# Kernel optimization log

Measured on AMD Instinct MI355X. Metric: run time of the kernel, lower is better.

## Reference

```python
import jax, jax.numpy as jnp
import numpy as np

DN = ('NHWC', 'HWIO', 'NHWC')
EPS = 1e-3  # Keras BatchNormalization default epsilon


def conv2d(x, w):
    return jax.lax.conv_general_dilated(x, w, (1, 1), 'SAME', dimension_numbers=DN)


def hard_sigmoid(x):
    # Keras ConvLSTM2D default recurrent_activation
    return jnp.clip(0.2 * x + 0.5, 0.0, 1.0)


def convlstm2d(x, Wx, Wh, b):
    """Keras ConvLSTM2D, return_sequences=True. x: (B,T,H,W,C).
    Wx: (3,3,C,4F) input kernel, Wh: (3,3,F,4F) recurrent kernel, b: (4F,).
    Gate order (Keras): i, f, c, o."""
    B, T, H, W, C = x.shape
    F = Wh.shape[2]
    # input-to-gate convs for all timesteps in one batched conv
    xg = conv2d(x.reshape(B * T, H, W, C), Wx) + b          # (B*T,H,W,4F)
    xg = xg.reshape(B, T, H, W, 4 * F).transpose(1, 0, 2, 3, 4)  # (T,B,H,W,4F)

    def step(carry, xg_t):
        h, c = carry
        g = xg_t + conv2d(h, Wh)                            # (B,H,W,4F)
        i, f, cc, o = jnp.split(g, 4, axis=-1)
        i = hard_sigmoid(i)
        f = hard_sigmoid(f)
        o = hard_sigmoid(o)
        c = f * c + i * jnp.tanh(cc)
        h = o * jnp.tanh(c)
        return (h, c), h

    h0 = jnp.zeros((B, H, W, F), x.dtype)
    (_, _), hs = jax.lax.scan(step, (h0, h0), xg)           # hs: (T,B,H,W,F)
    return hs.transpose(1, 0, 2, 3, 4)


def batchnorm(x, gamma, beta):
    # training-mode BN over all axes except channel (last)
    mu = x.mean(axis=(0, 1, 2, 3), keepdims=True)
    var = x.var(axis=(0, 1, 2, 3), keepdims=True)
    return gamma * (x - mu) * jax.lax.rsqrt(var + EPS) + beta


def setup_inputs() -> dict:
    key = jax.random.key(0)
    B, T, H, W, C = 4, 8, 16, 16, 256
    F = 256
    ks = jax.random.split(key, 10)
    s = 0.02
    inp = {
        'input_tensor': jax.random.normal(ks[0], (B, T, H, W, C), jnp.float32),
        'Wx1': jax.random.normal(ks[1], (3, 3, C, 4 * F), jnp.float32) * s,
        'Wh1': jax.random.normal(ks[2], (3, 3, F, 4 * F), jnp.float32) * s,
        'b1': jnp.zeros((4 * F,), jnp.float32),
        'g1': jnp.ones((F,), jnp.float32),
        'be1': jnp.zeros((F,), jnp.float32),
        'Wx2': jax.random.normal(ks[3], (3, 3, F, 4 * F), jnp.float32) * s,
        'Wh2': jax.random.normal(ks[4], (3, 3, F, 4 * F), jnp.float32) * s,
        'b2': jnp.zeros((4 * F,), jnp.float32),
        'g2': jnp.ones((F,), jnp.float32),
        'be2': jnp.zeros((F,), jnp.float32),
        'Wx3': jax.random.normal(ks[5], (3, 3, F, 4 * F), jnp.float32) * s,
        'Wh3': jax.random.normal(ks[6], (3, 3, F, 4 * F), jnp.float32) * s,
        'b3': jnp.zeros((4 * F,), jnp.float32),
        'g3': jnp.ones((F,), jnp.float32),
        'be3': jnp.zeros((F,), jnp.float32),
    }
    return inp


def reference(input_tensor, Wx1, Wh1, b1, g1, be1,
              Wx2, Wh2, b2, g2, be2,
              Wx3, Wh3, b3, g3, be3):
    x = batchnorm(convlstm2d(input_tensor, Wx1, Wh1, b1), g1, be1)
    x = batchnorm(convlstm2d(x, Wx2, Wh2, b2), g2, be2)
    x = batchnorm(convlstm2d(x, Wx3, Wh3, b3), g3, be3)
    return x
```

## Files before the change

kernel.cpp:

```cpp
#include <hip/hip_runtime.h>

#define HW      256
#define COUT    1024
#define TSTEPS  8
#define BN_EPS  1e-3f
#define KTOT    2304

typedef unsigned short u16;
typedef unsigned int   u32;
typedef __attribute__((ext_vector_type(8))) _Float16 v8h;
typedef __attribute__((ext_vector_type(4))) float v4f;

__device__ __forceinline__ u16 f2h(float x) {
    _Float16 h = (_Float16)x; return *(u16*)&h;
}
__device__ __forceinline__ float h2f(u16 u) {
    _Float16 h = *(_Float16*)&u; return (float)h;
}
__device__ __forceinline__ float hsig(float x) {
    return fminf(fmaxf(0.2f * x + 0.5f, 0.f), 1.f);
}

typedef __attribute__((address_space(1))) const unsigned int gas_u32;
typedef __attribute__((address_space(3))) unsigned int las_u32;
__device__ __forceinline__ void gl16(const void* g, void* l) {
    __builtin_amdgcn_global_load_lds((gas_u32*)g, (las_u32*)l, 16, 0, 0);
}

__global__ __launch_bounds__(256, 2) void conv_big_k(
    const u16* __restrict__ apad,
    const u16* __restrict__ wT,
    const float* __restrict__ bias,
    u16* __restrict__ out)
{
    constexpr int KQ = 36;
    __shared__ u16 lds[2 * 16384];

    const int bid = blockIdx.x;
    const int xcd = bid & 7, idx = bid >> 3;
    const int by = (xcd >> 1) * 2 + (idx & 1);
    const int bx = (xcd & 1) * 32 + (idx >> 1);
    const int m0 = bx * 128, n0 = by * 128;
    const int tid = threadIdx.x, lane = tid & 63, w = tid >> 6;
    const int wr = w >> 1, wc = w & 1;
    const int lr = lane >> 3;
    const int g  = (lane & 7) ^ lr;
    const int fr = lane & 15, kc = lane >> 4;

    const char* a_src[4];
    #pragma unroll
    for (int i = 0; i < 4; ++i) {
        int m = m0 + w * 32 + i * 8 + lr;
        int img = m >> 8, pix = m & 255, yy = pix >> 4, xx = pix & 15;
        a_src[i] = (const char*)apad + ((((long)img * 18 + yy) * 18 + xx) * 256 + g * 8) * 2;
    }
    const char* b_src[4];
    #pragma unroll
    for (int i = 0; i < 4; ++i) {
        int n = n0 + w * 32 + i * 8 + lr;
        b_src[i] = (const char*)wT + ((long)n * KTOT + g * 8) * 2;
    }

    int aro[4][2], bro[4][2];
    #pragma unroll
    for (int mi = 0; mi < 4; ++mi) {
        int rl = wr * 64 + mi * 16 + fr;
        #pragma unroll
        for (int ks = 0; ks < 2; ++ks)
            aro[mi][ks] = rl * 128 + ((((ks << 2) | kc) ^ (fr & 7)) << 4);
    }
    #pragma unroll
    for (int ni = 0; ni < 4; ++ni) {
        int nr = wc * 64 + ni * 16 + fr;
        #pragma unroll
        for (int ks = 0; ks < 2; ++ks)
            bro[ni][ks] = 16384 + nr * 128 + ((((ks << 2) | kc) ^ (fr & 7)) << 4);
    }

    v4f acc[4][4];
    #pragma unroll
    for (int mi = 0; mi < 4; ++mi)
        #pragma unroll
        for (int ni = 0; ni < 4; ++ni) acc[mi][ni] = (v4f)0.f;

#define STAGE_B(J) { int j_ = (J); int dxy = j_ >> 2, c64 = j_ & 3;           \
    int dy = (dxy * 11) >> 5; int dx = dxy - dy * 3;                          \
    int aoff = ((dy * 18 + dx) * 256 + c64 * 64) * 2; int boff = j_ * 128;    \
    char* base = (char*)lds + (j_ & 1) * 32768;                               \
    _Pragma("unroll") for (int i = 0; i < 4; ++i)                             \
        gl16(a_src[i] + aoff, base + (w * 32 + i * 8) * 128);                 \
    _Pragma("unroll") for (int i = 0; i < 4; ++i)                             \
        gl16(b_src[i] + boff, base + 16384 + (w * 32 + i * 8) * 128); }

#define COMPUTE_B(J) { const char* base = (const char*)lds + ((J) & 1) * 32768; \
    v8h af[4][2], bf[4][2];                                                   \
    _Pragma("unroll") for (int mi = 0; mi < 4; ++mi)                          \
        _Pragma("unroll") for (int ks = 0; ks < 2; ++ks)                      \
            af[mi][ks] = *(const v8h*)(base + aro[mi][ks]);                   \
    _Pragma("unroll") for (int ni = 0; ni < 4; ++ni)                          \
        _Pragma("unroll") for (int ks = 0; ks < 2; ++ks)                      \
            bf[ni][ks] = *(const v8h*)(base + bro[ni][ks]);                   \
    __builtin_amdgcn_s_setprio(1);                                            \
    _Pragma("unroll") for (int ks = 0; ks < 2; ++ks)                          \
    _Pragma("unroll") for (int mi = 0; mi < 4; ++mi)                          \
    _Pragma("unroll") for (int ni = 0; ni < 4; ++ni)                          \
        acc[mi][ni] = __builtin_amdgcn_mfma_f32_16x16x32_f16(af[mi][ks], bf[ni][ks], acc[mi][ni], 0, 0, 0); \
    __builtin_amdgcn_s_setprio(0); }

    STAGE_B(0);
    for (int kq = 0; kq < KQ - 1; ++kq) {
        asm volatile("s_waitcnt vmcnt(0)" ::: "memory");
        __builtin_amdgcn_s_barrier();
        __builtin_amdgcn_sched_barrier(0);
        STAGE_B(kq + 1);
        COMPUTE_B(kq);
    }
    asm volatile("s_waitcnt vmcnt(0)" ::: "memory");
    __builtin_amdgcn_s_barrier();
    __builtin_amdgcn_sched_barrier(0);
    COMPUTE_B(KQ - 1);
#undef STAGE_B
#undef COMPUTE_B

    #pragma unroll
    for (int mi = 0; mi < 4; ++mi) {
        #pragma unroll
        for (int ni = 0; ni < 4; ++ni) {
            int mrow = m0 + wr * 64 + mi * 16 + ((lane >> 4) << 2);
            int ncol = n0 + wc * 64 + ni * 16 + fr;
            float b0 = bias[(ncol & 3) * 256 + (ncol >> 2)];
            #pragma unroll
            for (int r = 0; r < 4; ++r)
                out[(long)(mrow + r) * COUT + ncol] = f2h(acc[mi][ni][r] + b0);
        }
    }
}

__global__ __launch_bounds__(512) void rec_fused_k(
    const u16* __restrict__ ph_in,
    const u16* __restrict__ wTf,
    const u16* __restrict__ xg,
    float* __restrict__ cbuf,
    float* __restrict__ hs,
    u16* __restrict__ ph_out,
    int t)
{
    __shared__ u16 lds[4 * 4096];

    const int bid = blockIdx.x;
    const int by = (bid & 7) * 2 + ((bid >> 3) & 1);
    const int bx = bid >> 4;
    const int m0 = bx * 64, n0 = by * 64;
    const int tid = threadIdx.x, lane = tid & 63, w = tid >> 6;
    const int wr = w >> 2, wc = w & 3;
    const int fr = lane & 15, kc = lane >> 4;

    const char* a_src;
    {
        int rt = tid >> 3;
        int gg = (tid & 7) ^ (rt & 7);
        int m = m0 + rt;
        int img = m >> 8, pix = m & 255, yy = pix >> 4, xx = pix & 15;
        a_src = (const char*)ph_in + ((((long)img * 18 + yy) * 18 + xx) * 256 + gg * 8) * 2;
    }
    const char* b_base = (const char*)wTf + ((long)(by * 4 + wc) * 72) * 1024 + lane * 16;

    int aro[2][2];
    #pragma unroll
    for (int mi = 0; mi < 2; ++mi)
        #pragma unroll
        for (int ks = 0; ks < 2; ++ks)
            aro[mi][ks] = (wr * 32 + mi * 16 + fr) * 128 + ((((ks << 2) | kc) ^ (fr & 7)) << 4);

    v4f acc0 = (v4f)0.f, acc1 = (v4f)0.f;

#define STAGE_A(J) { int j_ = (J); int dxy = j_ >> 2, c64 = j_ & 3;           \
    int dy = (dxy * 11) >> 5; int dx = dxy - dy * 3;                          \
    int aoff = ((dy * 18 + dx) * 256 + c64 * 64) * 2;                         \
    gl16(a_src + aoff, (char*)lds + (j_ & 3) * 8192 + w * 1024); }

#define LDB(J, R0, R1) { R0 = *(const v8h*)(b_base + (2 * (J)) * 1024);       \
                         R1 = *(const v8h*)(b_base + (2 * (J) + 1) * 1024); }

#define BODY(KQ, C0, C1, L0, L1) {                                            \
    int kq_ = (KQ); int jj_ = kq_ + 3 < 36 ? kq_ + 3 : 35;                    \
    asm volatile("s_waitcnt vmcnt(6)" ::: "memory");                          \
    __builtin_amdgcn_s_barrier();                                             \
    __builtin_amdgcn_sched_barrier(0);                                        \
    LDB(jj_, L0, L1);                                                         \
    STAGE_A(jj_);                                                             \
    const char* base_ = (const char*)lds + (kq_ & 3) * 8192;                  \
    v8h af00_ = *(const v8h*)(base_ + aro[0][0]);                             \
    v8h af10_ = *(const v8h*)(base_ + aro[1][0]);                             \
    v8h af01_ = *(const v8h*)(base_ + aro[0][1]);                             \
    v8h af11_ = *(const v8h*)(base_ + aro[1][1]);                             \
    __builtin_amdgcn_s_setprio(1);                                            \
    acc0 = __builtin_amdgcn_mfma_f32_16x16x32_f16(af00_, C0, acc0, 0, 0, 0);  \
    acc1 = __builtin_amdgcn_mfma_f32_16x16x32_f16(af10_, C0, acc1, 0, 0, 0);  \
    acc0 = __builtin_amdgcn_mfma_f32_16x16x32_f16(af01_, C1, acc0, 0, 0, 0);  \
    acc1 = __builtin_amdgcn_mfma_f32_16x16x32_f16(af11_, C1, acc1, 0, 0, 0);  \
    __builtin_amdgcn_s_setprio(0); }

    v8h S00, S01, S10, S11, S20, S21, S30, S31;
    LDB(0, S00, S01); STAGE_A(0);
    LDB(1, S10, S11); STAGE_A(1);
    LDB(2, S20, S21); STAGE_A(2);
    for (int j = 0; j < 9; ++j) {
        int k0 = 4 * j;
        BODY(k0,     S00, S01, S30, S31);
        BODY(k0 + 1, S10, S11, S00, S01);
        BODY(k0 + 2, S20, S21, S10, S11);
        BODY(k0 + 3, S30, S31, S20, S21);
    }
#undef STAGE_A
#undef LDB
#undef BODY

    v4f accA[2] = {acc0, acc1};
    const bool gl0 = lane & 1, gl1 = lane & 2;
    #pragma unroll
    for (int mi = 0; mi < 2; ++mi) {
        float V0 = accA[mi][0], V1 = accA[mi][1];
        float V2 = accA[mi][2], V3 = accA[mi][3];
        float x0 = __shfl_xor(V0, 1), x1 = __shfl_xor(V1, 1);
        float x2 = __shfl_xor(V2, 1), x3 = __shfl_xor(V3, 1);
        float a0 = gl0 ? x1 : V0;
        float a1 = gl0 ? V1 : x0;
        float a2 = gl0 ? x3 : V2;
        float a3 = gl0 ? V3 : x2;
        float s0 = __shfl_xor(a0, 2), s1 = __shfl_xor(a1, 2);
        float s2 = __shfl_xor(a2, 2), s3 = __shfl_xor(a3, 2);
        float Ti = gl1 ? s2 : a0;
        float Tf = gl1 ? s3 : a1;
        float Tc = gl1 ? a2 : s0;
        float To = gl1 ? a3 : s1;

        int row = m0 + wr * 32 + mi * 16 + ((lane >> 4) << 2) + (lane & 3);
        int f4  = n0 + wc * 16 + (lane & 12);
        int img = row >> 8, pix = row & 255, fch = f4 >> 2;
        long xrow = ((long)(img * TSTEPS + t) * HW + pix);
        uint2 xb = *(const uint2*)&xg[xrow * COUT + f4];
        float pi = Ti + h2f((u16)(xb.x & 0xffff));
        float pf = Tf + h2f((u16)(xb.x >> 16));
        float pc = Tc + h2f((u16)(xb.y & 0xffff));
        float po = To + h2f((u16)(xb.y >> 16));
        long cidx = (long)row * 256 + fch;
        float c = hsig(pf) * cbuf[cidx] + hsig(pi) * tanhf(pc);
        float h = hsig(po) * tanhf(c);
        cbuf[cidx] = c;
        hs[xrow * 256 + fch] = h;
        int yy = pix >> 4, xx = pix & 15;
        ph_out[(((long)img * 18 + yy + 1) * 18 + xx + 1) * 256 + fch] = f2h(h);
    }
}

__global__ __launch_bounds__(256) void gates0_k(
    const u16* __restrict__ xg, float* __restrict__ cbuf,
    float* __restrict__ hs, u16* __restrict__ ph_out)
{
    int idx = blockIdx.x * 256 + threadIdx.x;
    int fch = idx & 255, row = idx >> 8;
    int img = row >> 8, pix = row & 255;
    long xrow = (long)(img * TSTEPS) * HW + pix;
    uint2 xb = *(const uint2*)&xg[xrow * COUT + fch * 4];
    float pi = h2f((u16)(xb.x & 0xffff));
    float pc = h2f((u16)(xb.y & 0xffff));
    float po = h2f((u16)(xb.y >> 16));
    float c = hsig(pi) * tanhf(pc);
    float h = hsig(po) * tanhf(c);
    cbuf[(long)row * 256 + fch] = c;
    hs[xrow * 256 + fch] = h;
    int yy = pix >> 4, xx = pix & 15;
    ph_out[(((long)img * 18 + yy + 1) * 18 + xx + 1) * 256 + fch] = f2h(h);
}

__global__ __launch_bounds__(256) void wprep_k(const float* __restrict__ w,
                                               u16* __restrict__ wT)
{
    int k0 = blockIdx.x * 32;
    int np = blockIdx.y * 256 + threadIdx.x;
    int n  = (np & 3) * 256 + (np >> 2);
    u32 pk[16];
    #pragma unroll
    for (int kk = 0; kk < 32; kk += 2) {
        float a = w[(long)(k0 + kk) * COUT + n];
        float b = w[(long)(k0 + kk + 1) * COUT + n];
        pk[kk >> 1] = (u32)f2h(a) | ((u32)f2h(b) << 16);
    }
    uint4* dst = (uint4*)&wT[(long)np * KTOT + k0];
    dst[0] = make_uint4(pk[0], pk[1], pk[2], pk[3]);
    dst[1] = make_uint4(pk[4], pk[5], pk[6], pk[7]);
    dst[2] = make_uint4(pk[8], pk[9], pk[10], pk[11]);
    dst[3] = make_uint4(pk[12], pk[13], pk[14], pk[15]);
}

__global__ __launch_bounds__(256) void wprep_frag_k(const float* __restrict__ w,
                                                    u16* __restrict__ wTf)
{
    int kq = blockIdx.x;
    int nf = blockIdx.y * 4 + (threadIdx.x >> 6);
    int l  = threadIdx.x & 63;
    int np = nf * 16 + (l & 15);
    int n  = (np & 3) * 256 + (np >> 2);
    int k0 = kq * 32 + (l >> 4) * 8;
    u32 pk[4];
    #pragma unroll
    for (int e = 0; e < 8; e += 2) {
        float a = w[(long)(k0 + e) * COUT + n];
        float b = w[(long)(k0 + e + 1) * COUT + n];
        pk[e >> 1] = (u32)f2h(a) | ((u32)f2h(b) << 16);
    }
    *(uint4*)&wTf[((long)(nf * 72) + kq) * 512 + l * 8] =
        make_uint4(pk[0], pk[1], pk[2], pk[3]);
}

__global__ __launch_bounds__(256) void convert_x_k(const float* __restrict__ x,
                                                   u16* __restrict__ padx)
{
    int q = blockIdx.x * 256 + threadIdx.x;
    int e0 = q * 4;
    int f = e0 & 255, pix = (e0 >> 8) & 255, img = e0 >> 16;
    float4 v = ((const float4*)x)[q];
    int yy = pix >> 4, xx = pix & 15;
    long o = (((long)img * 18 + yy + 1) * 18 + xx + 1) * 256 + f;
    u32 lo = (u32)f2h(v.x) | ((u32)f2h(v.y) << 16);
    u32 hi = (u32)f2h(v.z) | ((u32)f2h(v.w) << 16);
    *(uint2*)&padx[o] = make_uint2(lo, hi);
}

__global__ __launch_bounds__(256) void bn_stats1_k(
    const float* __restrict__ x, float* __restrict__ partial)
{
    const int tid = threadIdx.x;
    const int blk = blockIdx.x;
    float s = 0.f, s2 = 0.f;
    const long base = (long)blk * 128 * 256;
    #pragma unroll 8
    for (int gi = 0; gi < 128; ++gi) {
        float v = x[base + gi * 256 + tid];
        s += v; s2 += v * v;
    }
    partial[blk * 512 + tid]       = s;
    partial[blk * 512 + 256 + tid] = s2;
}

__global__ __launch_bounds__(256) void bn_stats2_k(
    const float* __restrict__ partial, const float* __restrict__ gamma,
    const float* __restrict__ beta, float* __restrict__ stats)
{
    const int f = threadIdx.x;
    float s = 0.f, s2 = 0.f;
    #pragma unroll 8
    for (int b = 0; b < 64; ++b) {
        s  += partial[b * 512 + f];
        s2 += partial[b * 512 + 256 + f];
    }
    const float inv_n = 1.f / 8192.f;
    float mu  = s * inv_n;
    float var = s2 * inv_n - mu * mu;
    float sc  = gamma[f] * rsqrtf(var + BN_EPS);
    stats[f]       = sc;
    stats[256 + f] = beta[f] - mu * sc;
}

__global__ __launch_bounds__(256) void bn_apply_k(
    const float* __restrict__ x, const float* __restrict__ stats,
    u16* __restrict__ padx, float* __restrict__ out)
{
    const int q = blockIdx.x * 256 + threadIdx.x;
    const int e0 = q * 4;
    const int f = e0 & 255, pix = (e0 >> 8) & 255, img = e0 >> 16;
    float4 v  = ((const float4*)x)[q];
    float4 sc = *(const float4*)(stats + f);
    float4 sh = *(const float4*)(stats + 256 + f);
    v.x = v.x * sc.x + sh.x;
    v.y = v.y * sc.y + sh.y;
    v.z = v.z * sc.z + sh.z;
    v.w = v.w * sc.w + sh.w;
    if (out) ((float4*)out)[q] = v;
    if (padx) {
        int yy = pix >> 4, xx = pix & 15;
        long o = (((long)img * 18 + yy + 1) * 18 + xx + 1) * 256 + f;
        u32 lo = (u32)f2h(v.x) | ((u32)f2h(v.y) << 16);
        u32 hi = (u32)f2h(v.z) | ((u32)f2h(v.w) << 16);
        *(uint2*)&padx[o] = make_uint2(lo, hi);
    }
}

extern "C" void kernel_launch(void* const* d_in, const int* in_sizes, int n_in,
                              void* d_out, int out_size, void* d_ws, size_t ws_size,
                              hipStream_t stream)
{
    const float* x0    = (const float*)d_in[0];
    const float* Wx[3] = {(const float*)d_in[1], (const float*)d_in[6],  (const float*)d_in[11]};
    const float* Wh[3] = {(const float*)d_in[2], (const float*)d_in[7],  (const float*)d_in[12]};
    const float* bb[3] = {(const float*)d_in[3], (const float*)d_in[8],  (const float*)d_in[13]};
    const float* gg[3] = {(const float*)d_in[4], (const float*)d_in[9],  (const float*)d_in[14]};
    const float* be[3] = {(const float*)d_in[5], (const float*)d_in[10], (const float*)d_in[15]};

    float* ws    = (float*)d_ws;
    u16*  xg     = (u16*)ws;
    float* cbuf  = ws   + 4194304;
    float* hs    = cbuf + 262144;
    float* part  = hs   + 2097152;
    float* stats = part + 262144;
    u16*  pad_x  = (u16*)(stats + 512);
    u16*  pad_h  = pad_x + 2654208;
    u16*  wTx    = pad_h + 663552;
    u16*  wTf    = wTx   + 2359296;
    const long PHN = 331776;

    hipMemsetAsync(pad_x, 0, 2654208 * sizeof(u16), stream);
    hipMemsetAsync(pad_h, 0, 2 * PHN * sizeof(u16), stream);
    hipLaunchKernelGGL(convert_x_k, dim3(2048), dim3(256), 0, stream, x0, pad_x);

    for (int l = 0; l < 3; ++l) {
        hipLaunchKernelGGL(wprep_k, dim3(72, 4), dim3(256), 0, stream, Wx[l], wTx);
        hipLaunchKernelGGL(wprep_frag_k, dim3(72, 16), dim3(256), 0, stream, Wh[l], wTf);

        hipLaunchKernelGGL(conv_big_k, dim3(512), dim3(256), 0, stream,
            pad_x, wTx, bb[l], xg);

        hipLaunchKernelGGL(gates0_k, dim3(1024), dim3(256), 0, stream,
            xg, cbuf, hs, pad_h + PHN);

        for (int t = 1; t < TSTEPS; ++t) {
            hipLaunchKernelGGL(rec_fused_k, dim3(256), dim3(512), 0, stream,
                pad_h + (t & 1) * PHN, wTf, xg, cbuf, hs,
                pad_h + ((t & 1) ^ 1) * PHN, t);
        }

        hipLaunchKernelGGL(bn_stats1_k, dim3(64), dim3(256), 0, stream, hs, part);
        hipLaunchKernelGGL(bn_stats2_k, dim3(1), dim3(256), 0, stream, part, gg[l], be[l], stats);
        hipLaunchKernelGGL(bn_apply_k, dim3(2048), dim3(256), 0, stream, hs, stats,
            (l < 2) ? pad_x : (u16*)nullptr, (l == 2) ? (float*)d_out : (float*)nullptr);
    }
}
```

Baseline: 470.9 us.

## Deepen recurrent kernel pipeline to paired k-steps, prefetch xg, merge weight prep

The recurrent fused kernel now processes two k-slices per barrier using six LDS buffers instead of four. This halves the number of barriers per step and allows deeper prefetch of A tiles and B fragments. The xg gate-input load for the epilogue is issued before the main loop so its latency overlaps the GEMM. The two weight-preparation kernels are merged into one launch to cut launch overhead. The cost is more LDS and registers per block, which could reduce occupancy.

```diff
diff --git a/kernel.cpp b/kernel.cpp
--- a/kernel.cpp
+++ b/kernel.cpp
@@ -145,7 +145,7 @@
     u16* __restrict__ ph_out,
     int t)
 {
-    __shared__ u16 lds[4 * 4096];
+    __shared__ u16 lds[6 * 4096];
 
     const int bid = blockIdx.x;
     const int by = (bid & 7) * 2 + ((bid >> 3) & 1);
@@ -155,6 +155,18 @@
     const int wr = w >> 2, wc = w & 3;
     const int fr = lane & 15, kc = lane >> 4;
 
+    const int f4  = n0 + wc * 16 + (lane & 12);
+    const int fch = f4 >> 2;
+    int erow[2]; long xrow[2];
+    uint2 xb_pre[2];
+    #pragma unroll
+    for (int mi = 0; mi < 2; ++mi) {
+        erow[mi] = m0 + wr * 32 + mi * 16 + ((lane >> 4) << 2) + (lane & 3);
+        int img = erow[mi] >> 8, pix = erow[mi] & 255;
+        xrow[mi] = ((long)(img * TSTEPS + t) * HW + pix);
+        xb_pre[mi] = *(const uint2*)&xg[xrow[mi] * COUT + f4];
+    }
+
     const char* a_src;
     {
         int rt = tid >> 3;
@@ -174,22 +186,16 @@
 
     v4f acc0 = (v4f)0.f, acc1 = (v4f)0.f;
 
-#define STAGE_A(J) { int j_ = (J); int dxy = j_ >> 2, c64 = j_ & 3;           \
+#define STAGE_A(J, BUF) { int j_ = (J); int dxy = j_ >> 2, c64 = j_ & 3;      \
     int dy = (dxy * 11) >> 5; int dx = dxy - dy * 3;                          \
     int aoff = ((dy * 18 + dx) * 256 + c64 * 64) * 2;                         \
-    gl16(a_src + aoff, (char*)lds + (j_ & 3) * 8192 + w * 1024); }
+    gl16(a_src + aoff, (char*)lds + (BUF) * 8192 + w * 1024); }
 
 #define LDB(J, R0, R1) { R0 = *(const v8h*)(b_base + (2 * (J)) * 1024);       \
                          R1 = *(const v8h*)(b_base + (2 * (J) + 1) * 1024); }
 
-#define BODY(KQ, C0, C1, L0, L1) {                                            \
-    int kq_ = (KQ); int jj_ = kq_ + 3 < 36 ? kq_ + 3 : 35;                    \
-    asm volatile("s_waitcnt vmcnt(6)" ::: "memory");                          \
-    __builtin_amdgcn_s_barrier();                                             \
-    __builtin_amdgcn_sched_barrier(0);                                        \
-    LDB(jj_, L0, L1);                                                         \
-    STAGE_A(jj_);                                                             \
-    const char* base_ = (const char*)lds + (kq_ & 3) * 8192;                  \
+#define CKQ(BUF, C0, C1) {                                                    \
+    const char* base_ = (const char*)lds + (BUF) * 8192;                      \
     v8h af00_ = *(const v8h*)(base_ + aro[0][0]);                             \
     v8h af10_ = *(const v8h*)(base_ + aro[1][0]);                             \
     v8h af01_ = *(const v8h*)(base_ + aro[0][1]);                             \
@@ -201,20 +207,40 @@
     acc1 = __builtin_amdgcn_mfma_f32_16x16x32_f16(af11_, C1, acc1, 0, 0, 0);  \
     __builtin_amdgcn_s_setprio(0); }
 
-    v8h S00, S01, S10, S11, S20, S21, S30, S31;
-    LDB(0, S00, S01); STAGE_A(0);
-    LDB(1, S10, S11); STAGE_A(1);
-    LDB(2, S20, S21); STAGE_A(2);
-    for (int j = 0; j < 9; ++j) {
-        int k0 = 4 * j;
-        BODY(k0,     S00, S01, S30, S31);
-        BODY(k0 + 1, S10, S11, S00, S01);
-        BODY(k0 + 2, S20, S21, S10, S11);
-        BODY(k0 + 3, S30, S31, S20, S21);
-    }
+#define BODY2(J2, BC, BS, Ca0, Ca1, Cb0, Cb1, La0, La1, Lb0, Lb1) {           \
+    int q0_ = 2 * (J2);                                                       \
+    asm volatile("s_waitcnt vmcnt(6)" ::: "memory");                          \
+    __builtin_amdgcn_s_barrier();                                             \
+    __builtin_amdgcn_sched_barrier(0);                                        \
+    LDB(q0_ + 4, La0, La1); LDB(q0_ + 5, Lb0, Lb1);                           \
+    STAGE_A(q0_ + 4, BS); STAGE_A(q0_ + 5, (BS) + 1);                         \
+    CKQ(BC,       Ca0, Ca1);                                                  \
+    CKQ((BC) + 1, Cb0, Cb1); }
+
+    v8h S00, S01, S02, S03, S10, S11, S12, S13, S20, S21, S22, S23;
+    LDB(0, S00, S01); LDB(1, S02, S03); STAGE_A(0, 0); STAGE_A(1, 1);
+    LDB(2, S10, S11); LDB(3, S12, S13); STAGE_A(2, 2); STAGE_A(3, 3);
+
+    for (int j = 0; j < 5; ++j) {
+        BODY2(3 * j,     0, 4, S00, S01, S02, S03, S20, S21, S22, S23);
+        BODY2(3 * j + 1, 2, 0, S10, S11, S12, S13, S00, S01, S02, S03);
+        BODY2(3 * j + 2, 4, 2, S20, S21, S22, S23, S10, S11, S12, S13);
+    }
+    BODY2(15, 0, 4, S00, S01, S02, S03, S20, S21, S22, S23);
+    asm volatile("s_waitcnt vmcnt(6)" ::: "memory");
+    __builtin_amdgcn_s_barrier();
+    __builtin_amdgcn_sched_barrier(0);
+    CKQ(2, S10, S11);
+    CKQ(3, S12, S13);
+    asm volatile("s_waitcnt vmcnt(0)" ::: "memory");
+    __builtin_amdgcn_s_barrier();
+    __builtin_amdgcn_sched_barrier(0);
+    CKQ(4, S20, S21);
+    CKQ(5, S22, S23);
 #undef STAGE_A
 #undef LDB
-#undef BODY
+#undef CKQ
+#undef BODY2
 
     v4f accA[2] = {acc0, acc1};
     const bool gl0 = lane & 1, gl1 = lane & 2;
@@ -235,22 +261,17 @@
         float Tc = gl1 ? a2 : s0;
         float To = gl1 ? a3 : s1;
 
-        int row = m0 + wr * 32 + mi * 16 + ((lane >> 4) << 2) + (lane & 3);
-        int f4  = n0 + wc * 16 + (lane & 12);
-        int img = row >> 8, pix = row & 255, fch = f4 >> 2;
-        long xrow = ((long)(img * TSTEPS + t) * HW + pix);
-        uint2 xb = *(const uint2*)&xg[xrow * COUT + f4];
-        float pi = Ti + h2f((u16)(xb.x & 0xffff));
-        float pf = Tf + h2f((u16)(xb.x >> 16));
-        float pc = Tc + h2f((u16)(xb.y & 0xffff));
-        float po = To + h2f((u16)(xb.y >> 16));
-        long cidx = (long)row * 256 + fch;
+        float pi = Ti + h2f((u16)(xb_pre[mi].x & 0xffff));
+        float pf = Tf + h2f((u16)(xb_pre[mi].x >> 16));
+        float pc = Tc + h2f((u16)(xb_pre[mi].y & 0xffff));
+        float po = To + h2f((u16)(xb_pre[mi].y >> 16));
+        long cidx = (long)erow[mi] * 256 + fch;
         float c = hsig(pf) * cbuf[cidx] + hsig(pi) * tanhf(pc);
         float h = hsig(po) * tanhf(c);
         cbuf[cidx] = c;
-        hs[xrow * 256 + fch] = h;
-        int yy = pix >> 4, xx = pix & 15;
-        ph_out[(((long)img * 18 + yy + 1) * 18 + xx + 1) * 256 + fch] = f2h(h);
+        hs[xrow[mi] * 256 + fch] = h;
+        int pix = erow[mi] & 255, img = erow[mi] >> 8;
+        ph_out[(((long)img * 18 + (pix >> 4) + 1) * 18 + (pix & 15) + 1) * 256 + fch] = f2h(h);
     }
 }
 
@@ -274,44 +295,44 @@
     ph_out[(((long)img * 18 + yy + 1) * 18 + xx + 1) * 256 + fch] = f2h(h);
 }
 
-__global__ __launch_bounds__(256) void wprep_k(const float* __restrict__ w,
-                                               u16* __restrict__ wT)
-{
-    int k0 = blockIdx.x * 32;
-    int np = blockIdx.y * 256 + threadIdx.x;
-    int n  = (np & 3) * 256 + (np >> 2);
-    u32 pk[16];
-    #pragma unroll
-    for (int kk = 0; kk < 32; kk += 2) {
-        float a = w[(long)(k0 + kk) * COUT + n];
-        float b = w[(long)(k0 + kk + 1) * COUT + n];
-        pk[kk >> 1] = (u32)f2h(a) | ((u32)f2h(b) << 16);
-    }
-    uint4* dst = (uint4*)&wT[(long)np * KTOT + k0];
-    dst[0] = make_uint4(pk[0], pk[1], pk[2], pk[3]);
-    dst[1] = make_uint4(pk[4], pk[5], pk[6], pk[7]);
-    dst[2] = make_uint4(pk[8], pk[9], pk[10], pk[11]);
-    dst[3] = make_uint4(pk[12], pk[13], pk[14], pk[15]);
-}
-
-__global__ __launch_bounds__(256) void wprep_frag_k(const float* __restrict__ w,
-                                                    u16* __restrict__ wTf)
+__global__ __launch_bounds__(256) void wprep_all_k(
+    const float* __restrict__ wx, const float* __restrict__ wh,
+    u16* __restrict__ wT, u16* __restrict__ wTf)
 {
     int kq = blockIdx.x;
-    int nf = blockIdx.y * 4 + (threadIdx.x >> 6);
-    int l  = threadIdx.x & 63;
-    int np = nf * 16 + (l & 15);
-    int n  = (np & 3) * 256 + (np >> 2);
-    int k0 = kq * 32 + (l >> 4) * 8;
-    u32 pk[4];
-    #pragma unroll
-    for (int e = 0; e < 8; e += 2) {
-        float a = w[(long)(k0 + e) * COUT + n];
-        float b = w[(long)(k0 + e + 1) * COUT + n];
-        pk[e >> 1] = (u32)f2h(a) | ((u32)f2h(b) << 16);
-    }
-    *(uint4*)&wTf[((long)(nf * 72) + kq) * 512 + l * 8] =
-        make_uint4(pk[0], pk[1], pk[2], pk[3]);
+    int by = blockIdx.y;
+    if (by < 4) {
+        int k0 = kq * 32;
+        int np = by * 256 + threadIdx.x;
+        int n  = (np & 3) * 256 + (np >> 2);
+        u32 pk[16];
+        #pragma unroll
+        for (int kk = 0; kk < 32; kk += 2) {
+            float a = wx[(long)(k0 + kk) * COUT + n];
+            float b = wx[(long)(k0 + kk + 1) * COUT + n];
+            pk[kk >> 1] = (u32)f2h(a) | ((u32)f2h(b) << 16);
+        }
+        uint4* dst = (uint4*)&wT[(long)np * KTOT + k0];
+        dst[0] = make_uint4(pk[0], pk[1], pk[2], pk[3]);
+        dst[1] = make_uint4(pk[4], pk[5], pk[6], pk[7]);
+        dst[2] = make_uint4(pk[8], pk[9], pk[10], pk[11]);
+        dst[3] = make_uint4(pk[12], pk[13], pk[14], pk[15]);
+    } else {
+        int nf = (by - 4) * 4 + (threadIdx.x >> 6);
+        int l  = threadIdx.x & 63;
+        int np = nf * 16 + (l & 15);
+        int n  = (np & 3) * 256 + (np >> 2);
+        int k0 = kq * 32 + (l >> 4) * 8;
+        u32 pk[4];
+        #pragma unroll
+        for (int e = 0; e < 8; e += 2) {
+            float a = wh[(long)(k0 + e) * COUT + n];
+            float b = wh[(long)(k0 + e + 1) * COUT + n];
+            pk[e >> 1] = (u32)f2h(a) | ((u32)f2h(b) << 16);
+        }
+        *(uint4*)&wTf[((long)(nf * 72) + kq) * 512 + l * 8] =
+            make_uint4(pk[0], pk[1], pk[2], pk[3]);
+    }
 }
 
 __global__ __launch_bounds__(256) void convert_x_k(const float* __restrict__ x,
@@ -415,8 +436,8 @@
     hipLaunchKernelGGL(convert_x_k, dim3(2048), dim3(256), 0, stream, x0, pad_x);
 
     for (int l = 0; l < 3; ++l) {
-        hipLaunchKernelGGL(wprep_k, dim3(72, 4), dim3(256), 0, stream, Wx[l], wTx);
-        hipLaunchKernelGGL(wprep_frag_k, dim3(72, 16), dim3(256), 0, stream, Wh[l], wTf);
+        hipLaunchKernelGGL(wprep_all_k, dim3(72, 20), dim3(256), 0, stream,
+            Wx[l], Wh[l], wTx, wTf);
 
         hipLaunchKernelGGL(conv_big_k, dim3(512), dim3(256), 0, stream,
             pad_x, wTx, bb[l], xg);
```

Measured after the change: 471.3 us. Within noise of the previous version (+0.1%).
